# Kernel optimization log

Measured on AMD Instinct MI355X. Metric: run time of the kernel, lower is better.

The kernel has to match this reference:

```python
import jax, jax.numpy as jnp
import numpy as np

D = 1024  # input_size
NORM = 1.0 / np.sqrt(D)


def setup_inputs() -> dict:
    key = jax.random.key(0)
    k_x, k_q, k_k, k_v = jax.random.split(key, 4)
    B, S = 4, 2048
    scale = 1.0 / np.sqrt(D)  # init ~ nn.Linear default magnitude
    return {
        "inputs": jax.random.normal(k_x, (B, S, D), dtype=jnp.float32),
        "Wq": jax.random.uniform(k_q, (D, D), jnp.float32, -scale, scale),
        "Wk": jax.random.uniform(k_k, (D, D), jnp.float32, -scale, scale),
        "Wv": jax.random.uniform(k_v, (D, D), jnp.float32, -scale, scale),
    }


def reference(inputs, Wq, Wk, Wv):
    # nn.Linear(x) = x @ W.T (no bias)
    Q = jnp.einsum("bsd,ed->bse", inputs, Wq)
    K = jnp.einsum("bsd,ed->bse", inputs, Wk)
    V = jnp.einsum("bsd,ed->bse", inputs, Wv)
    attn = jnp.einsum("bqe,bke->bqk", Q, K) * NORM  # [B,S,S]
    attn = jax.nn.softmax(attn, axis=2)
    return jnp.einsum("bqk,bke->bqe", attn, V)
```

## Files before the change

### kernel.cpp

```cpp
#include <hip/hip_runtime.h>

typedef __bf16 bf16_t;
typedef __bf16 bf16x8 __attribute__((ext_vector_type(8)));
typedef __bf16 bf16x4 __attribute__((ext_vector_type(4)));
typedef float  floatx4 __attribute__((ext_vector_type(4)));

__device__ __forceinline__ void gload_lds16(const bf16_t* g, bf16_t* l) {
    __builtin_amdgcn_global_load_lds(
        (const __attribute__((address_space(1))) void*)g,
        (__attribute__((address_space(3))) void*)l,
        16, 0, 0);
}

__device__ __forceinline__ bf16x8 ds_read_b128f(const bf16_t* l) {
    bf16x8 r;
    asm volatile("ds_read_b128 %0, %1"
        : "=v"(r)
        : "v"((const __attribute__((address_space(3))) bf16_t*)l));
    return r;
}

template <int MODE, int BN, int MAP, typename OutT>
__global__ __launch_bounds__(512, 2) void gemm8p(
    const bf16_t* __restrict__ A, int lda, size_t batchA,
    const bf16_t* __restrict__ B, int ldb, size_t batchB,
    OutT* __restrict__ C, int ldc, size_t batchC,
    bf16_t* __restrict__ C2,
    float* __restrict__ rowsums, int batchR,
    int K, float scale)
{
    extern __shared__ __align__(16) bf16_t smem[];

    constexpr int NJ   = BN / 64;
    constexpr int WCB  = BN / 4;
    constexpr int BGL  = BN / 128;
    constexpr int AREG = 8192;
    constexpr int BREG = BN * 32;
    constexpr int BOFF = 2 * AREG;
    constexpr int BUFS = BOFF + 2 * BREG;
    constexpr int VM   = 2 + 2 * BGL;

    int bxL, byL, bzL;
    if constexpr (MAP == 1) {
        const int h = blockIdx.x, k = h & 7, s = h >> 3;
        bzL = k >> 1; bxL = ((k & 1) << 2) | (s & 3); byL = s >> 2;
    } else if constexpr (MAP == 2) {
        const int h = blockIdx.x, k = h & 7, s = h >> 3;
        bzL = 0; bxL = s >> 3; byL = (k << 3) | (s & 7);
    } else {
        bxL = blockIdx.x; byL = blockIdx.y; bzL = blockIdx.z;
    }

    A += (size_t)bzL * batchA;
    B += (size_t)bzL * batchB;

    const int tid  = threadIdx.x;
    const int wid  = tid >> 6;
    const int lane = tid & 63;
    const int wr   = wid >> 2;
    const int wc   = wid & 3;
    const int lr   = lane & 15;

    const int bm = bxL * 256;
    const int bn = byL * BN;

    const bf16_t* At = A + (size_t)bm * lda;
    const bf16_t* Bt = B + (size_t)bn * ldb;

    const int    c8 = (((lane & 3) ^ ((lane >> 3) & 3)) << 3);
    const size_t ga = (size_t)(wid * 16 + (lane >> 2)) * lda + c8;
    const size_t gb = (size_t)(wid * 16 + (lane >> 2)) * ldb + c8;

    const int slotoff = (((lane >> 4) ^ ((lr >> 1) & 3)) << 3);

    const int NT = K >> 6;

    floatx4 acc[8][NJ] = {};
    bf16x8 af[4], bq[NJ];

#define RBASE(sbuf, sreg)                                                     \
    ((sbuf) * BUFS + ((sreg) < 2 ? (sreg) * AREG : BOFF + ((sreg) - 2) * BREG))

#define STAGE(sbuf, sreg, tile) do {                                          \
    bf16_t* _l = smem + RBASE(sbuf, sreg) + (wid << 9);                       \
    const size_t _k = (size_t)(tile) * 64 + ((sreg) & 1) * 32;                \
    if ((sreg) >= 2) {                                                        \
        gload_lds16(Bt + _k + gb, _l);                                        \
        if (BGL == 2)                                                         \
            gload_lds16(Bt + _k + gb + (size_t)128 * ldb, _l + 4096);         \
    } else {                                                                  \
        gload_lds16(At + _k + ga, _l);                                        \
        gload_lds16(At + _k + ga + (size_t)128 * lda, _l + 4096);             \
    }                                                                         \
} while (0)

#define PHASE(buf, kk, mh, RDB, sbuf, sreg, stile, DOVM) do {                 \
    if (RDB) {                                                                \
        _Pragma("unroll")                                                     \
        for (int j = 0; j < NJ; ++j)                                          \
            bq[j] = ds_read_b128f(&smem[(buf) * BUFS + BOFF + (kk) * BREG +   \
                        ((wc * WCB + j * 16 + lr) << 5) + slotoff]);          \
    }                                                                         \
    _Pragma("unroll")                                                         \
    for (int i = 0; i < 4; ++i)                                               \
        af[i] = ds_read_b128f(&smem[(buf) * BUFS + (kk) * AREG +              \
                    ((wr * 128 + (mh) * 64 + i * 16 + lr) << 5) + slotoff]);  \
    STAGE(sbuf, sreg, stile);                                                 \
    if (DOVM) {                                                               \
        if constexpr (VM == 6) asm volatile("s_waitcnt vmcnt(6)" ::: "memory");\
        else                   asm volatile("s_waitcnt vmcnt(4)" ::: "memory");\
    }                                                                         \
    __builtin_amdgcn_s_barrier();                                             \
    asm volatile("s_waitcnt lgkmcnt(0)" ::: "memory");                        \
    __builtin_amdgcn_sched_barrier(0);                                        \
    __builtin_amdgcn_s_setprio(1);                                            \
    _Pragma("unroll")                                                         \
    for (int i = 0; i < 4; ++i) {                                             \
        _Pragma("unroll")                                                     \
        for (int j = 0; j < NJ; ++j)                                          \
            acc[(mh) * 4 + i][j] = __builtin_amdgcn_mfma_f32_16x16x32_bf16(   \
                bq[j], af[i], acc[(mh) * 4 + i][j], 0, 0, 0);                 \
    }                                                                         \
    __builtin_amdgcn_s_setprio(0);                                            \
    __builtin_amdgcn_s_barrier();                                             \
} while (0)

    STAGE(0, 2, 0); STAGE(0, 0, 0); STAGE(0, 3, 0); STAGE(0, 1, 0);
    STAGE(1, 2, 1); STAGE(1, 0, 1); STAGE(1, 3, 1);
    if constexpr (VM == 6) asm volatile("s_waitcnt vmcnt(6)" ::: "memory");
    else                   asm volatile("s_waitcnt vmcnt(4)" ::: "memory");
    __builtin_amdgcn_s_barrier();

    for (int kt = 0; kt < NT; kt += 2) {
        int t1 = kt + 1;
        int t2 = kt + 2; if (t2 >= NT) t2 -= NT;
        int t3 = kt + 3; if (t3 >= NT) t3 -= NT;
        PHASE(0, 0, 0, 1,  1, 1, t1, 0);
        PHASE(0, 0, 1, 0,  0, 2, t2, 0);
        PHASE(0, 1, 0, 1,  0, 0, t2, 0);
        PHASE(0, 1, 1, 0,  0, 3, t2, 1);
        PHASE(1, 0, 0, 1,  0, 1, t2, 0);
        PHASE(1, 0, 1, 0,  1, 2, t3, 0);
        PHASE(1, 1, 0, 1,  1, 0, t3, 0);
        PHASE(1, 1, 1, 0,  1, 3, t3, 1);
    }
    asm volatile("s_waitcnt vmcnt(0)" ::: "memory");

#undef PHASE
#undef STAGE
#undef RBASE

    const int cfix = lane & 15;
    const int creg = (lane >> 4) << 2;

    if constexpr (MODE == 1) {
        OutT* Cz = C + (size_t)bzL * batchC;
        #pragma unroll
        for (int mi = 0; mi < 8; ++mi) {
            size_t row = (size_t)(bm + wr * 128 + mi * 16 + cfix);
            #pragma unroll
            for (int j = 0; j < NJ; ++j) {
                int col = bn + wc * WCB + j * 16 + creg;
                bf16x4 v;
                #pragma unroll
                for (int r = 0; r < 4; ++r) v[r] = (bf16_t)acc[mi][j][r];
                *(bf16x4*)&Cz[row * (size_t)ldc + col] = v;
            }
        }
    } else if constexpr (MODE == 5) {
        bf16_t* dst = (bn < 1024) ? (bf16_t*)C : C2;
        const int cb = bn & 1023;
        #pragma unroll
        for (int mi = 0; mi < 8; ++mi) {
            size_t row = (size_t)(bm + wr * 128 + mi * 16 + cfix);
            #pragma unroll
            for (int j = 0; j < NJ; ++j) {
                int col = cb + wc * WCB + j * 16 + creg;
                bf16x4 v;
                #pragma unroll
                for (int r = 0; r < 4; ++r) v[r] = (bf16_t)acc[mi][j][r];
                *(bf16x4*)&dst[row * (size_t)ldc + col] = v;
            }
        }
    } else if constexpr (MODE == 2) {
        OutT* Cz = C + (size_t)bzL * batchC;
        float* sums = rowsums + (size_t)bzL * batchR;
        float rs[8] = {};
        #pragma unroll
        for (int mi = 0; mi < 8; ++mi) {
            size_t row = (size_t)(bm + wr * 128 + mi * 16 + cfix);
            #pragma unroll
            for (int j = 0; j < NJ; ++j) {
                int col = bn + wc * WCB + j * 16 + creg;
                bf16x4 v;
                #pragma unroll
                for (int r = 0; r < 4; ++r) {
                    v[r] = (bf16_t)__expf(acc[mi][j][r] * scale);
                    rs[mi] += (float)v[r];
                }
                *(bf16x4*)&Cz[row * (size_t)ldc + col] = v;
            }
        }
        #pragma unroll
        for (int mi = 0; mi < 8; ++mi) {
            rs[mi] += __shfl_xor(rs[mi], 16);
            rs[mi] += __shfl_xor(rs[mi], 32);
        }
        if (lane < 16) {
            #pragma unroll
            for (int mi = 0; mi < 8; ++mi)
                atomicAdd(&sums[bm + wr * 128 + mi * 16 + lane], rs[mi]);
        }
    } else {
        OutT* Cz = C + (size_t)bzL * batchC;
        const float* sums = rowsums + (size_t)bzL * batchR;
        #pragma unroll
        for (int mi = 0; mi < 8; ++mi) {
            int rloc = bm + wr * 128 + mi * 16 + cfix;
            float rinv = 1.0f / sums[rloc];
            size_t row = (size_t)rloc;
            #pragma unroll
            for (int j = 0; j < NJ; ++j) {
                int col = bn + wc * WCB + j * 16 + creg;
                floatx4 v;
                #pragma unroll
                for (int r = 0; r < 4; ++r) v[r] = acc[mi][j][r] * rinv;
                *(floatx4*)&Cz[row * (size_t)ldc + col] = v;
            }
        }
    }
}

__global__ __launch_bounds__(256) void cvt_all(
    const float* __restrict__ X, const float* __restrict__ Wq,
    const float* __restrict__ Wk, const float* __restrict__ Wv,
    bf16_t* __restrict__ Xb, bf16_t* __restrict__ Wqb,
    bf16_t* __restrict__ Wkb, bf16_t* __restrict__ Wvb,
    float* __restrict__ sums, int nsums,
    int nX4, int nW4)
{
    int i = blockIdx.x * blockDim.x + threadIdx.x;
    if (i < nsums) sums[i] = 0.f;
    const float* src; bf16_t* dst; int idx;
    if (i < nX4) { src = X; dst = Xb; idx = i; }
    else {
        int j = i - nX4;
        int w = j / nW4;
        idx = j - w * nW4;
        if (i >= nX4 + 3 * nW4) return;
        src = (w == 0) ? Wq : (w == 1) ? Wk : Wv;
        dst = (w == 0) ? Wqb : (w == 1) ? Wkb : Wvb;
    }
    float4 v = ((const float4*)src)[idx];
    bf16x4 o;
    o[0] = (bf16_t)v.x; o[1] = (bf16_t)v.y; o[2] = (bf16_t)v.z; o[3] = (bf16_t)v.w;
    *(bf16x4*)(dst + (size_t)idx * 4) = o;
}

extern "C" void kernel_launch(void* const* d_in, const int* in_sizes, int n_in,
                              void* d_out, int out_size, void* d_ws, size_t ws_size,
                              hipStream_t stream)
{
    (void)in_sizes; (void)n_in; (void)out_size; (void)ws_size;
    const float* X  = (const float*)d_in[0];
    const float* Wq = (const float*)d_in[1];
    const float* Wk = (const float*)d_in[2];
    const float* Wv = (const float*)d_in[3];
    float* out = (float*)d_out;

    const int Bb = 4, S = 2048, D = 1024;
    const int M = Bb * S;

    char* ws = (char*)d_ws;
    size_t off = 0;
    auto carve = [&](size_t bytes) -> char* {
        char* p = ws + off;
        off += (bytes + 255) & ~(size_t)255;
        return p;
    };
    bf16_t* Xb  = (bf16_t*)carve((size_t)M * D * 2);
    bf16_t* Wqb = (bf16_t*)carve((size_t)D * D * 2);
    bf16_t* Wkb = (bf16_t*)carve((size_t)D * D * 2);
    bf16_t* Wvb = (bf16_t*)carve((size_t)D * D * 2);
    bf16_t* Qb  = (bf16_t*)carve((size_t)M * D * 2);
    bf16_t* Kb  = (bf16_t*)carve((size_t)M * D * 2);
    bf16_t* Vt  = (bf16_t*)carve((size_t)D * M * 2);
    bf16_t* Sc  = (bf16_t*)carve((size_t)Bb * S * S * 2);
    float*  sums = (float*)carve((size_t)M * 4);

    static bool s_attr = false;
    if (!s_attr) {
        (void)hipFuncSetAttribute(
            reinterpret_cast<const void*>(&gemm8p<5, 256, 0, bf16_t>),
            hipFuncAttributeMaxDynamicSharedMemorySize, 131072);
        (void)hipFuncSetAttribute(
            reinterpret_cast<const void*>(&gemm8p<2, 256, 1, bf16_t>),
            hipFuncAttributeMaxDynamicSharedMemorySize, 131072);
        (void)hipFuncSetAttribute(
            reinterpret_cast<const void*>(&gemm8p<1, 128, 2, bf16_t>),
            hipFuncAttributeMaxDynamicSharedMemorySize, 98304);
        (void)hipFuncSetAttribute(
            reinterpret_cast<const void*>(&gemm8p<3, 128, 1, float>),
            hipFuncAttributeMaxDynamicSharedMemorySize, 98304);
        s_attr = true;
    }

    const int nX4 = M * D / 4, nW4 = D * D / 4;
    const int tot4 = nX4 + 3 * nW4;
    cvt_all<<<(tot4 + 255) / 256, 256, 0, stream>>>(
        X, Wq, Wk, Wv, Xb, Wqb, Wkb, Wvb, sums, M, nX4, nW4);

    gemm8p<5, 256, 0, bf16_t><<<dim3(M / 256, (2 * D) / 256, 1), 512, 131072, stream>>>(
        Xb, D, 0, Wqb, D, 0, Qb, D, 0, Kb, nullptr, 0, D, 1.0f);

    gemm8p<1, 128, 2, bf16_t><<<dim3(256, 1, 1), 512, 98304, stream>>>(
        Wvb, D, 0, Xb, D, 0, Vt, M, 0, nullptr, nullptr, 0, D, 1.0f);

    gemm8p<2, 256, 1, bf16_t><<<dim3(256, 1, 1), 512, 131072, stream>>>(
        Qb, D, (size_t)S * D, Kb, D, (size_t)S * D, Sc, S, (size_t)S * S,
        nullptr, sums, S, D, 0.03125f);

    gemm8p<3, 128, 1, float><<<dim3(256, 1, 1), 512, 98304, stream>>>(
        Sc, S, (size_t)S * S, Vt, M, (size_t)S, out, D, (size_t)S * D,
        nullptr, sums, S, S, 1.0f);
}
```

Before: 232.5 us.

## Fuse conversion and four GEMM stages into one persistent kernel with grid barriers

Replaces the five separate launches (conversion, QK projection, V projection, scores, output) with one persistent 256-block kernel. Stages are separated by software grid barriers built on atomic counters, and each stage is reached through a shared device gemm_core function. The aim is to remove launch gaps and per-kernel ramp-up and tail costs. In exchange the barrier spins and needs all 256 blocks co-resident, and it breaks out after a fixed spin count, which risks reading incomplete data. The conversion phase also now runs on only 256 blocks, and the kernel uses the larger 128KB shared-memory footprint in every stage.

```diff
diff --git a/kernel.cpp b/kernel.cpp
--- a/kernel.cpp
+++ b/kernel.cpp
@@ -20,17 +20,33 @@
     return r;
 }
 
+__device__ __forceinline__ void gridbar(unsigned* ctr) {
+    __syncthreads();
+    if (threadIdx.x == 0) {
+        __threadfence();
+        __hip_atomic_fetch_add(ctr, 1u, __ATOMIC_ACQ_REL,
+                               __HIP_MEMORY_SCOPE_AGENT);
+        int spins = 0;
+        while (__hip_atomic_load(ctr, __ATOMIC_RELAXED,
+                                 __HIP_MEMORY_SCOPE_AGENT) < 256u) {
+            __builtin_amdgcn_s_sleep(16);
+            if (++spins > (1 << 21)) break;
+        }
+    }
+    __syncthreads();
+    __threadfence();
+}
+
 template <int MODE, int BN, int MAP, typename OutT>
-__global__ __launch_bounds__(512, 2) void gemm8p(
-    const bf16_t* __restrict__ A, int lda, size_t batchA,
-    const bf16_t* __restrict__ B, int ldb, size_t batchB,
-    OutT* __restrict__ C, int ldc, size_t batchC,
-    bf16_t* __restrict__ C2,
-    float* __restrict__ rowsums, int batchR,
-    int K, float scale)
+__device__ __forceinline__ void gemm_core(
+    int h,
+    const bf16_t* A, int lda, size_t batchA,
+    const bf16_t* B, int ldb, size_t batchB,
+    OutT* C, int ldc, size_t batchC,
+    bf16_t* C2,
+    float* rowsums, int batchR,
+    int K, float scale, bf16_t* smem)
 {
-    extern __shared__ __align__(16) bf16_t smem[];
-
     constexpr int NJ   = BN / 64;
     constexpr int WCB  = BN / 4;
     constexpr int BGL  = BN / 128;
@@ -42,13 +58,13 @@
 
     int bxL, byL, bzL;
     if constexpr (MAP == 1) {
-        const int h = blockIdx.x, k = h & 7, s = h >> 3;
+        const int k = h & 7, s = h >> 3;
         bzL = k >> 1; bxL = ((k & 1) << 2) | (s & 3); byL = s >> 2;
     } else if constexpr (MAP == 2) {
-        const int h = blockIdx.x, k = h & 7, s = h >> 3;
+        const int k = h & 7, s = h >> 3;
         bzL = 0; bxL = s >> 3; byL = (k << 3) | (s & 7);
     } else {
-        bxL = blockIdx.x; byL = blockIdx.y; bzL = blockIdx.z;
+        bxL = h & 31; byL = h >> 5; bzL = 0;
     }
 
     A += (size_t)bzL * batchA;
@@ -217,7 +233,9 @@
         #pragma unroll
         for (int mi = 0; mi < 8; ++mi) {
             int rloc = bm + wr * 128 + mi * 16 + cfix;
-            float rinv = 1.0f / sums[rloc];
+            float sv = __hip_atomic_load(&sums[rloc], __ATOMIC_RELAXED,
+                                         __HIP_MEMORY_SCOPE_AGENT);
+            float rinv = 1.0f / sv;
             size_t row = (size_t)rloc;
             #pragma unroll
             for (int j = 0; j < NJ; ++j) {
@@ -231,30 +249,58 @@
     }
 }
 
-__global__ __launch_bounds__(256) void cvt_all(
+__global__ __launch_bounds__(512, 2) void mega_attn(
     const float* __restrict__ X, const float* __restrict__ Wq,
     const float* __restrict__ Wk, const float* __restrict__ Wv,
-    bf16_t* __restrict__ Xb, bf16_t* __restrict__ Wqb,
-    bf16_t* __restrict__ Wkb, bf16_t* __restrict__ Wvb,
-    float* __restrict__ sums, int nsums,
+    bf16_t* Xb, bf16_t* Wqb, bf16_t* Wkb, bf16_t* Wvb,
+    bf16_t* Qb, bf16_t* Kb, bf16_t* Vt, bf16_t* Sc,
+    float* sums, float* out, unsigned* bar,
     int nX4, int nW4)
 {
-    int i = blockIdx.x * blockDim.x + threadIdx.x;
-    if (i < nsums) sums[i] = 0.f;
-    const float* src; bf16_t* dst; int idx;
-    if (i < nX4) { src = X; dst = Xb; idx = i; }
-    else {
-        int j = i - nX4;
-        int w = j / nW4;
-        idx = j - w * nW4;
-        if (i >= nX4 + 3 * nW4) return;
-        src = (w == 0) ? Wq : (w == 1) ? Wk : Wv;
-        dst = (w == 0) ? Wqb : (w == 1) ? Wkb : Wvb;
-    }
-    float4 v = ((const float4*)src)[idx];
-    bf16x4 o;
-    o[0] = (bf16_t)v.x; o[1] = (bf16_t)v.y; o[2] = (bf16_t)v.z; o[3] = (bf16_t)v.w;
-    *(bf16x4*)(dst + (size_t)idx * 4) = o;
+    extern __shared__ __align__(16) bf16_t smem[];
+    const int h   = blockIdx.x;
+    const int tid = threadIdx.x;
+    const int S = 2048, D = 1024, M = 8192;
+
+    {
+        const int gtid = h * 512 + tid;
+        const int tot4 = nX4 + 3 * nW4;
+        for (int i = gtid; i < tot4; i += 131072) {
+            const float* src; bf16_t* dst; int idx;
+            if (i < nX4) { src = X; dst = Xb; idx = i; }
+            else {
+                int j = i - nX4;
+                int w = j / nW4;
+                idx = j - w * nW4;
+                src = (w == 0) ? Wq : (w == 1) ? Wk : Wv;
+                dst = (w == 0) ? Wqb : (w == 1) ? Wkb : Wvb;
+            }
+            float4 v = ((const float4*)src)[idx];
+            bf16x4 o;
+            o[0] = (bf16_t)v.x; o[1] = (bf16_t)v.y;
+            o[2] = (bf16_t)v.z; o[3] = (bf16_t)v.w;
+            *(bf16x4*)(dst + (size_t)idx * 4) = o;
+        }
+        if (gtid < M) sums[gtid] = 0.f;
+    }
+    gridbar(bar + 0);
+
+    gemm_core<5, 256, 3, bf16_t>(h, Xb, D, 0, Wqb, D, 0,
+                                 Qb, D, 0, Kb, nullptr, 0, D, 1.0f, smem);
+    gridbar(bar + 16);
+
+    gemm_core<1, 128, 2, bf16_t>(h, Wvb, D, 0, Xb, D, 0,
+                                 Vt, M, 0, nullptr, nullptr, 0, D, 1.0f, smem);
+    gridbar(bar + 32);
+
+    gemm_core<2, 256, 1, bf16_t>(h, Qb, D, (size_t)S * D, Kb, D, (size_t)S * D,
+                                 Sc, S, (size_t)S * S, nullptr,
+                                 sums, S, D, 0.03125f, smem);
+    gridbar(bar + 48);
+
+    gemm_core<3, 128, 1, float>(h, Sc, S, (size_t)S * S, Vt, M, (size_t)S,
+                                out, D, (size_t)S * D, nullptr,
+                                sums, S, S, 1.0f, smem);
 }
 
 extern "C" void kernel_launch(void* const* d_in, const int* in_sizes, int n_in,
@@ -287,40 +333,20 @@
     bf16_t* Vt  = (bf16_t*)carve((size_t)D * M * 2);
     bf16_t* Sc  = (bf16_t*)carve((size_t)Bb * S * S * 2);
     float*  sums = (float*)carve((size_t)M * 4);
+    unsigned* bar = (unsigned*)carve(256);
 
     static bool s_attr = false;
     if (!s_attr) {
         (void)hipFuncSetAttribute(
-            reinterpret_cast<const void*>(&gemm8p<5, 256, 0, bf16_t>),
+            reinterpret_cast<const void*>(&mega_attn),
             hipFuncAttributeMaxDynamicSharedMemorySize, 131072);
-        (void)hipFuncSetAttribute(
-            reinterpret_cast<const void*>(&gemm8p<2, 256, 1, bf16_t>),
-            hipFuncAttributeMaxDynamicSharedMemorySize, 131072);
-        (void)hipFuncSetAttribute(
-            reinterpret_cast<const void*>(&gemm8p<1, 128, 2, bf16_t>),
-            hipFuncAttributeMaxDynamicSharedMemorySize, 98304);
-        (void)hipFuncSetAttribute(
-            reinterpret_cast<const void*>(&gemm8p<3, 128, 1, float>),
-            hipFuncAttributeMaxDynamicSharedMemorySize, 98304);
         s_attr = true;
     }
 
+    (void)hipMemsetAsync(bar, 0, 256, stream);
+
     const int nX4 = M * D / 4, nW4 = D * D / 4;
-    const int tot4 = nX4 + 3 * nW4;
-    cvt_all<<<(tot4 + 255) / 256, 256, 0, stream>>>(
-        X, Wq, Wk, Wv, Xb, Wqb, Wkb, Wvb, sums, M, nX4, nW4);
-
-    gemm8p<5, 256, 0, bf16_t><<<dim3(M / 256, (2 * D) / 256, 1), 512, 131072, stream>>>(
-        Xb, D, 0, Wqb, D, 0, Qb, D, 0, Kb, nullptr, 0, D, 1.0f);
-
-    gemm8p<1, 128, 2, bf16_t><<<dim3(256, 1, 1), 512, 98304, stream>>>(
-        Wvb, D, 0, Xb, D, 0, Vt, M, 0, nullptr, nullptr, 0, D, 1.0f);
-
-    gemm8p<2, 256, 1, bf16_t><<<dim3(256, 1, 1), 512, 131072, stream>>>(
-        Qb, D, (size_t)S * D, Kb, D, (size_t)S * D, Sc, S, (size_t)S * S,
-        nullptr, sums, S, D, 0.03125f);
-
-    gemm8p<3, 128, 1, float><<<dim3(256, 1, 1), 512, 98304, stream>>>(
-        Sc, S, (size_t)S * S, Vt, M, (size_t)S, out, D, (size_t)S * D,
-        nullptr, sums, S, S, 1.0f);
-}
+    mega_attn<<<dim3(256, 1, 1), 512, 131072, stream>>>(
+        X, Wq, Wk, Wv, Xb, Wqb, Wkb, Wvb, Qb, Kb, Vt, Sc,
+        sums, out, bar, nX4, nW4);
+}
```

Result: slower. 407.6 us (+75.3%).
